# Kernel tuning notes

Measured on AMD Instinct MI355X. Metric: run time of the kernel, lower is better.

## Reference

```python
import jax, jax.numpy as jnp
import numpy as np

B, S, HID = 2, 2048, 2048
H, D = 16, 128
BASE = 10000.0
NEG = -1e9


def _rope_tables(seq_len, dim, dtype):
    inv_freq = 1.0 / (BASE ** (jnp.arange(0, dim, 2, dtype=jnp.float32) / dim))
    pos = jnp.arange(seq_len, dtype=jnp.float32)
    freqs = jnp.einsum('s,d->sd', pos, inv_freq)          # [S, D/2]
    emb = jnp.concatenate([freqs, freqs], axis=-1)        # [S, D]
    return jnp.cos(emb).astype(dtype), jnp.sin(emb).astype(dtype)


def _rotate_half(x):
    x1, x2 = jnp.split(x, 2, axis=-1)
    return jnp.concatenate([-x2, x1], axis=-1)


def setup_inputs() -> dict:
    key = jax.random.key(0)
    k1, k2, k3 = jax.random.split(key, 3)
    x = jax.random.normal(k1, (B, S, HID), dtype=jnp.float32)
    w_qkv = jax.random.normal(k2, (HID, 3 * HID), dtype=jnp.float32) * (HID ** -0.5)
    w_out = jax.random.normal(k3, (HID, HID), dtype=jnp.float32) * (HID ** -0.5)
    return {"x": x, "w_qkv": w_qkv, "w_out": w_out}


def reference(x, w_qkv, w_out):
    b, s, _ = x.shape
    qkv = x @ w_qkv                                        # [B, S, 3*HID]
    qkv = qkv.reshape(b, s, 3, H, D).transpose(2, 0, 3, 1, 4)  # [3, B, H, S, D]
    q, k, v = qkv[0], qkv[1], qkv[2]
    cos, sin = _rope_tables(s, D, x.dtype)                 # [S, D]
    cos = cos[None, None]
    sin = sin[None, None]
    q = q * cos + _rotate_half(q) * sin
    k = k * cos + _rotate_half(k) * sin
    scale = 1.0 / np.sqrt(D)
    scores = jnp.einsum('bhqd,bhkd->bhqk', q, k) * scale   # [B, H, S, S]
    causal = jnp.triu(jnp.ones((s, s), dtype=bool), k=1)
    scores = jnp.where(causal[None, None], NEG, scores)
    attn = jax.nn.softmax(scores, axis=-1)
    out = jnp.einsum('bhqk,bhkd->bhqd', attn, v)           # [B, H, S, D]
    out = out.transpose(0, 2, 1, 3).reshape(b, s, H * D)
    return out @ w_out
```

## Files before the change

### kernel.cpp

```cpp
#include <hip/hip_runtime.h>
#include <hip/hip_bf16.h>

#define S_LEN 2048
#define HID_DIM 2048
#define NH 16
#define HD 128
#define N3 6144

typedef __bf16 bf16x8 __attribute__((ext_vector_type(8)));
typedef unsigned short u16x8 __attribute__((ext_vector_type(8)));
typedef float f32x4 __attribute__((ext_vector_type(4)));
typedef float f32x16 __attribute__((ext_vector_type(16)));

#define MFMA16(a, b, c) __builtin_amdgcn_mfma_f32_16x16x32_bf16(a, b, c, 0, 0, 0)
#define MFMA32(a, b, c) __builtin_amdgcn_mfma_f32_32x32x16_bf16(a, b, c, 0, 0, 0)

__device__ __forceinline__ unsigned short f2bf(float f) {
  union { float f; unsigned u; } v; v.f = f;
  return (unsigned short)((v.u + 0x7fffu + ((v.u >> 16) & 1u)) >> 16);
}
__device__ __forceinline__ float bf2f(unsigned short h) {
  union { unsigned u; float f; } v; v.u = ((unsigned)h) << 16; return v.f;
}
__device__ __forceinline__ unsigned packbf2(float lo, float hi) {
  union { __hip_bfloat162 h2; unsigned u; } cv;
  cv.h2 = __float22bfloat162_rn(make_float2(lo, hi));
  return cv.u;
}
__device__ __forceinline__ void store_c(float* p, float v) { *p = v; }
__device__ __forceinline__ void store_c(unsigned short* p, float v) { *p = f2bf(v); }

__device__ __forceinline__ void async16(const void* g, void* l) {
  __builtin_amdgcn_global_load_lds((const __attribute__((address_space(1))) unsigned int*)g,
                                   (__attribute__((address_space(3))) unsigned int*)l,
                                   16, 0, 0);
}

template <int N> __device__ __forceinline__ void vmcnt();
template <> __device__ __forceinline__ void vmcnt<0>() { asm volatile("s_waitcnt vmcnt(0)" ::: "memory"); }
template <> __device__ __forceinline__ void vmcnt<5>() { asm volatile("s_waitcnt vmcnt(5)" ::: "memory"); }
template <> __device__ __forceinline__ void vmcnt<6>() { asm volatile("s_waitcnt vmcnt(6)" ::: "memory"); }

#define PLSWAP(a, b) asm volatile("v_permlane32_swap_b32 %0, %1" : "+v"(a), "+v"(b))

__global__ __launch_bounds__(256) void prep_all(const float4* __restrict__ x4,
                                                ushort4* __restrict__ xb4,
                                                const float* __restrict__ w_qkv,
                                                unsigned short* __restrict__ wqkvT,
                                                const float* __restrict__ w_out,
                                                unsigned short* __restrict__ woutT,
                                                float* __restrict__ cosT,
                                                float* __restrict__ sinT) {
  __shared__ float t[32][33];
  int bid = blockIdx.x;
  const int tid = threadIdx.x;

  if (bid < 8192) {
    int i = bid * 256 + tid;
    float4 v = x4[i];
    ushort4 o;
    o.x = f2bf(v.x); o.y = f2bf(v.y); o.z = f2bf(v.z); o.w = f2bf(v.w);
    xb4[i] = o;
    return;
  }
  bid -= 8192;
  if (bid < 12288 + 4096) {
    const float* src; unsigned short* dst; int R, Ccols;
    if (bid < 12288) { src = w_qkv; dst = wqkvT; R = 2048; Ccols = 6144; }
    else { bid -= 12288; src = w_out; dst = woutT; R = 2048; Ccols = 2048; }
    int ct = Ccols >> 5;
    int bx = bid % ct, by = bid / ct;
    int c0 = bx << 5, r0 = by << 5;
    int lx = tid & 31, ly = tid >> 5;
#pragma unroll
    for (int i = 0; i < 32; i += 8)
      t[ly + i][lx] = src[(long long)(r0 + ly + i) * Ccols + c0 + lx];
    __syncthreads();
#pragma unroll
    for (int i = 0; i < 32; i += 8)
      dst[(long long)(c0 + ly + i) * R + r0 + lx] = f2bf(t[lx][ly + i]);
    return;
  }
  bid -= 16384;
  int idx = bid * 256 + tid;
  int s = idx >> 6, i = idx & 63;
  float invf = powf(10000.0f, -(float)i * (1.0f / 64.0f));
  float a = (float)s * invf;
  cosT[idx] = cosf(a);
  sinT[idx] = sinf(a);
}

__global__ __launch_bounds__(512) void gemm256(const unsigned short* __restrict__ A,
                                               const unsigned short* __restrict__ Bt,
                                               unsigned short* __restrict__ C,
                                               int Mdim, int Ncols, int ldc, int Kdim) {
  constexpr int AEL = 256 * 64, BUFE = 2 * AEL;
  __shared__ unsigned short smem[2 * BUFE];

  const int ntn = Ncols >> 8;
  const int nwg = (Mdim >> 8) * ntn;
  int bid = blockIdx.x;
  bid = (bid & 7) * (nwg >> 3) + (bid >> 3);
  const int tm = (bid / ntn) << 8;
  const int tn = (bid % ntn) << 8;

  const int tid = threadIdx.x;
  const int w = tid >> 6, l = tid & 63;
  const int g = l >> 4, cc = l & 15;
  const int wm = w >> 2, wn = w & 3;

  const int srow = tid >> 3;
  const int schunk = (tid & 7) ^ (srow & 7);
  const unsigned short* gA = A + (long long)(tm + srow) * Kdim + schunk * 8;
  const unsigned short* gB = Bt + (long long)(tn + srow) * Kdim + schunk * 8;

  const int ch0 = ((g) ^ (cc & 7)) << 3;
  const int ch1 = ((4 + g) ^ (cc & 7)) << 3;

  f32x4 acc[8][4] = {};
  bf16x8 a[4][2], b[4][2];
  const int nk = Kdim >> 6;

#define ST_A(kt2, BUF, s) \
  async16(gA + (long long)(s) * 64 * Kdim + ((long long)(kt2) << 6), \
          smem + (BUF) * BUFE + (s) * 4096 + w * 512)
#define ST_B(kt2, BUF, s) \
  async16(gB + (long long)(s) * 64 * Kdim + ((long long)(kt2) << 6), \
          smem + (BUF) * BUFE + AEL + (s) * 4096 + w * 512)

#pragma unroll
  for (int s = 0; s < 4; ++s) ST_A(0, 0, s);
#pragma unroll
  for (int s = 0; s < 4; ++s) ST_B(0, 0, s);
  ST_A(1, 1, 0); ST_A(1, 1, 2);
  ST_B(1, 1, 0); ST_B(1, 1, 1); ST_B(1, 1, 2); ST_B(1, 1, 3);
  vmcnt<6>();
  __builtin_amdgcn_s_barrier();

#define KSTEP(kt, BUF, OBUF)                                                      \
  {                                                                               \
    const unsigned short* Ab = smem + (BUF) * BUFE + wm * (128 * 64);             \
    const unsigned short* Bb = smem + (BUF) * BUFE + AEL + wn * (64 * 64);        \
                    \
    _Pragma("unroll") for (int i = 0; i < 4; ++i) {                               \
      const int r = (i * 16 + cc) << 6;                                           \
      a[i][0] = *(const bf16x8*)(Ab + r + ch0);                                   \
      a[i][1] = *(const bf16x8*)(Ab + r + ch1);                                   \
    }                                                                             \
    _Pragma("unroll") for (int j = 0; j < 2; ++j) {                               \
      const int r = (j * 16 + cc) << 6;                                           \
      b[j][0] = *(const bf16x8*)(Bb + r + ch0);                                   \
      b[j][1] = *(const bf16x8*)(Bb + r + ch1);                                   \
    }                                                                             \
    if ((kt) + 1 < nk) { ST_A((kt) + 1, OBUF, 1); ST_A((kt) + 1, OBUF, 3); }      \
    __builtin_amdgcn_s_barrier();                                                 \
    __builtin_amdgcn_s_setprio(1);                                                \
    _Pragma("unroll") for (int i = 0; i < 4; ++i)                                 \
      _Pragma("unroll") for (int j = 0; j < 2; ++j) {                             \
        acc[i][j] = MFMA16(a[i][0], b[j][0], acc[i][j]);                          \
        acc[i][j] = MFMA16(a[i][1], b[j][1], acc[i][j]);                          \
      }                                                                           \
    __builtin_amdgcn_s_setprio(0);                                                \
    __builtin_amdgcn_s_barrier();                                                 \
                                              \
    _Pragma("unroll") for (int j = 0; j < 2; ++j) {                               \
      const int r = ((2 + j) * 16 + cc) << 6;                                     \
      b[2 + j][0] = *(const bf16x8*)(Bb + r + ch0);                               \
      b[2 + j][1] = *(const bf16x8*)(Bb + r + ch1);                               \
    }                                                                             \
    if ((kt) + 2 < nk) { ST_A((kt) + 2, BUF, 0); ST_A((kt) + 2, BUF, 2); }        \
    __builtin_amdgcn_s_barrier();                                                 \
    __builtin_amdgcn_s_setprio(1);                                                \
    _Pragma("unroll") for (int i = 0; i < 4; ++i)                                 \
      _Pragma("unroll") for (int j = 0; j < 2; ++j) {                             \
        acc[i][2 + j] = MFMA16(a[i][0], b[2 + j][0], acc[i][2 + j]);              \
        acc[i][2 + j] = MFMA16(a[i][1], b[2 + j][1], acc[i][2 + j]);              \
      }                                                                           \
    __builtin_amdgcn_s_setprio(0);                                                \
    __builtin_amdgcn_s_barrier();                                                 \
                                              \
    _Pragma("unroll") for (int i = 0; i < 4; ++i) {                               \
      const int r = ((64 + i * 16 + cc) << 6);                                    \
      a[i][0] = *(const bf16x8*)(Ab + r + ch0);                                   \
      a[i][1] = *(const bf16x8*)(Ab + r + ch1);                                   \
    }                                                                             \
    if ((kt) + 2 < nk) { ST_B((kt) + 2, BUF, 0); ST_B((kt) + 2, BUF, 1); }        \
    __builtin_amdgcn_s_barrier();                                                 \
    __builtin_amdgcn_s_setprio(1);                                                \
    _Pragma("unroll") for (int i = 0; i < 4; ++i)                                 \
      _Pragma("unroll") for (int j = 0; j < 2; ++j) {                             \
        acc[4 + i][j] = MFMA16(a[i][0], b[j][0], acc[4 + i][j]);                  \
        acc[4 + i][j] = MFMA16(a[i][1], b[j][1], acc[4 + i][j]);                  \
      }                                                                           \
    __builtin_amdgcn_s_setprio(0);                                                \
    __builtin_amdgcn_s_barrier();                                                 \
                            \
    if ((kt) + 2 < nk) { ST_B((kt) + 2, BUF, 2); ST_B((kt) + 2, BUF, 3); }        \
    __builtin_amdgcn_s_barrier();                                                 \
    __builtin_amdgcn_s_setprio(1);                                                \
    _Pragma("unroll") for (int i = 0; i < 4; ++i)                                 \
      _Pragma("unroll") for (int j = 0; j < 2; ++j) {                             \
        acc[4 + i][2 + j] = MFMA16(a[i][0], b[2 + j][0], acc[4 + i][2 + j]);      \
        acc[4 + i][2 + j] = MFMA16(a[i][1], b[2 + j][1], acc[4 + i][2 + j]);      \
      }                                                                           \
    __builtin_amdgcn_s_setprio(0);                                                \
    if ((kt) + 2 < nk) vmcnt<6>(); else vmcnt<0>();                               \
    __builtin_amdgcn_s_barrier();                                                 \
  }

  for (int kt = 0; kt < nk; kt += 2) {
    KSTEP(kt, 0, 1);
    KSTEP(kt + 1, 1, 0);
  }
#undef KSTEP
#undef ST_A
#undef ST_B

  const int crow0 = tm + wm * 128;
  const int ccol0 = tn + wn * 64;
#pragma unroll
  for (int i = 0; i < 8; ++i)
#pragma unroll
    for (int j = 0; j < 4; ++j)
#pragma unroll
      for (int p = 0; p < 4; ++p) {
        int row = crow0 + i * 16 + (g << 2) + p;
        int col = ccol0 + j * 16 + cc;
        store_c(&C[(long long)row * ldc + col], acc[i][j][p]);
      }
}

template <int BM, int BN, typename OutT>
__global__ __launch_bounds__(512) void gemm_pipe8(const unsigned short* __restrict__ A,
                                                  const unsigned short* __restrict__ Bt,
                                                  OutT* __restrict__ C,
                                                  int Mdim, int Ncols, int ldc, int Kdim) {
  constexpr int WTM = BM / 2, WTN = BN / 4;
  constexpr int MREP = WTM / 16, NREP = WTN / 16;
  constexpr int AEL = BM * 64, BEL = BN * 64, BUFE = AEL + BEL;
  constexpr int AINST = BM / 64, BINST = BN / 64;
  constexpr int AHALF = BM / 128, BHALF = BN / 128;
  constexpr int VN = BN / 64 + BM / 128;
  __shared__ unsigned short smem[2 * BUFE];

  const int ntn = Ncols / BN;
  const int nwg = (Mdim / BM) * ntn;
  int bid = blockIdx.x;
  bid = (bid & 7) * (nwg >> 3) + (bid >> 3);
  const int tm = (bid / ntn) * BM;
  const int tn = (bid % ntn) * BN;

  const int tid = threadIdx.x;
  const int w = tid >> 6, l = tid & 63;
  const int g = l >> 4, cc = l & 15;
  const int wm = w >> 2, wn = w & 3;

  const int srow = tid >> 3;
  const int schunk = (tid & 7) ^ (srow & 7);
  const unsigned short* gA = A + (long long)(tm + srow) * Kdim + schunk * 8;
  const unsigned short* gB = Bt + (long long)(tn + srow) * Kdim + schunk * 8;

  const int ch0 = ((g) ^ (cc & 7)) << 3;
  const int ch1 = ((4 + g) ^ (cc & 7)) << 3;

  f32x4 acc[MREP][NREP] = {};
  bf16x8 a[MREP / 2][2], b[NREP][2];

  const int nk = Kdim >> 6;

#define STAGE_A(kt2, s) \
  async16(gA + (long long)(s) * 64 * Kdim + ((long long)(kt2) << 6), \
          smem + ((kt2) & 1) * BUFE + (s) * 4096 + w * 512)
#define STAGE_B(kt2, s) \
  async16(gB + (long long)(s) * 64 * Kdim + ((long long)(kt2) << 6), \
          smem + ((kt2) & 1) * BUFE + AEL + (s) * 4096 + w * 512)

#pragma unroll
  for (int s = 0; s < AINST; ++s) STAGE_A(0, s);
#pragma unroll
  for (int s = 0; s < BINST; ++s) STAGE_B(0, s);
#pragma unroll
  for (int s = 0; s < BINST; ++s) STAGE_B(1, s);
#pragma unroll
  for (int s = 0; s < AHALF; ++s) STAGE_A(1, s);
  vmcnt<VN>();
  __builtin_amdgcn_s_barrier();

  for (int kt = 0; kt < nk; ++kt) {
    const int buf = kt & 1;
    const unsigned short* Ab = smem + buf * BUFE + (wm * WTM) * 64;
    const unsigned short* Bb = smem + buf * BUFE + AEL + (wn * WTN) * 64;

#pragma unroll
    for (int i = 0; i < MREP / 2; ++i) {
      const int r = (i * 16 + cc) << 6;
      a[i][0] = *(const bf16x8*)(Ab + r + ch0);
      a[i][1] = *(const bf16x8*)(Ab + r + ch1);
    }
#pragma unroll
    for (int j = 0; j < NREP; ++j) {
      const int r = (j * 16 + cc) << 6;
      b[j][0] = *(const bf16x8*)(Bb + r + ch0);
      b[j][1] = *(const bf16x8*)(Bb + r + ch1);
    }
    if (kt + 1 < nk) {
#pragma unroll
      for (int s = AHALF; s < AINST; ++s) STAGE_A(kt + 1, s);
    }
    __builtin_amdgcn_s_barrier();
    __builtin_amdgcn_s_setprio(1);
#pragma unroll
    for (int i = 0; i < MREP / 2; ++i)
#pragma unroll
      for (int j = 0; j < NREP / 2; ++j) {
        acc[i][j] = MFMA16(a[i][0], b[j][0], acc[i][j]);
        acc[i][j] = MFMA16(a[i][1], b[j][1], acc[i][j]);
      }
    __builtin_amdgcn_s_setprio(0);
    __builtin_amdgcn_s_barrier();

    if (kt + 2 < nk) {
#pragma unroll
      for (int s = 0; s < BHALF; ++s) STAGE_B(kt + 2, s);
    }
    __builtin_amdgcn_s_barrier();
    __builtin_amdgcn_s_setprio(1);
#pragma unroll
    for (int i = 0; i < MREP / 2; ++i)
#pragma unroll
      for (int j = 0; j < NREP / 2; ++j) {
        f32x4& ac = acc[i][NREP / 2 + j];
        ac = MFMA16(a[i][0], b[NREP / 2 + j][0], ac);
        ac = MFMA16(a[i][1], b[NREP / 2 + j][1], ac);
      }
    __builtin_amdgcn_s_setprio(0);
    __builtin_amdgcn_s_barrier();

#pragma unroll
    for (int i = 0; i < MREP / 2; ++i) {
      const int r = ((WTM / 2) + i * 16 + cc) << 6;
      a[i][0] = *(const bf16x8*)(Ab + r + ch0);
      a[i][1] = *(const bf16x8*)(Ab + r + ch1);
    }
    if (kt + 2 < nk) {
#pragma unroll
      for (int s = BHALF; s < BINST; ++s) STAGE_B(kt + 2, s);
    }
    __builtin_amdgcn_s_barrier();
    __builtin_amdgcn_s_setprio(1);
#pragma unroll
    for (int i = 0; i < MREP / 2; ++i)
#pragma unroll
      for (int j = 0; j < NREP / 2; ++j) {
        f32x4& ac = acc[MREP / 2 + i][j];
        ac = MFMA16(a[i][0], b[j][0], ac);
        ac = MFMA16(a[i][1], b[j][1], ac);
      }
    __builtin_amdgcn_s_setprio(0);
    __builtin_amdgcn_s_barrier();

    if (kt + 2 < nk) {
#pragma unroll
      for (int s = 0; s < AHALF; ++s) STAGE_A(kt + 2, s);
    }
    __builtin_amdgcn_s_barrier();
    __builtin_amdgcn_s_setprio(1);
#pragma unroll
    for (int i = 0; i < MREP / 2; ++i)
#pragma unroll
      for (int j = 0; j < NREP / 2; ++j) {
        f32x4& ac = acc[MREP / 2 + i][NREP / 2 + j];
        ac = MFMA16(a[i][0], b[NREP / 2 + j][0], ac);
        ac = MFMA16(a[i][1], b[NREP / 2 + j][1], ac);
      }
    __builtin_amdgcn_s_setprio(0);
    if (kt + 2 < nk) vmcnt<VN>(); else vmcnt<0>();
    __builtin_amdgcn_s_barrier();
  }
#undef STAGE_A
#undef STAGE_B

  const int crow0 = tm + wm * WTM;
  const int ccol0 = tn + wn * WTN;
#pragma unroll
  for (int i = 0; i < MREP; ++i)
#pragma unroll
    for (int j = 0; j < NREP; ++j)
#pragma unroll
      for (int p = 0; p < 4; ++p) {
        int row = crow0 + i * 16 + (g << 2) + p;
        int col = ccol0 + j * 16 + cc;
        store_c(&C[(long long)row * ldc + col], acc[i][j][p]);
      }
}

__global__ __launch_bounds__(256) void split_rope(const unsigned short* __restrict__ qkv,
                                                  const float* __restrict__ cosT,
                                                  const float* __restrict__ sinT,
                                                  unsigned short* __restrict__ Qb,
                                                  unsigned short* __restrict__ Kb,
                                                  unsigned short* __restrict__ Vt) {
  __shared__ unsigned short vtile[32][128];
  const int bid = blockIdx.x;
  const int st = bid & 63;
  const int h = (bid >> 6) & 15;
  const int b = bid >> 10;
  const int s0 = st << 5;
  const int t = threadIdx.x;
  const float qscale = 0.08838834764831845f;

  {
    const int sl = t >> 3;
    const int d0 = (t & 7) << 3;
    const int s = s0 + sl;
    const long long rb = ((long long)(b * S_LEN + s)) * N3 + h * HD;
    u16x8 qlo = *(const u16x8*)(qkv + rb + d0);
    u16x8 qhi = *(const u16x8*)(qkv + rb + 64 + d0);
    u16x8 klo = *(const u16x8*)(qkv + rb + HID_DIM + d0);
    u16x8 khi = *(const u16x8*)(qkv + rb + HID_DIM + 64 + d0);
    const float* cp = cosT + (s << 6) + d0;
    const float* sp = sinT + (s << 6) + d0;
    f32x4 c0 = *(const f32x4*)(cp), c1 = *(const f32x4*)(cp + 4);
    f32x4 sn0 = *(const f32x4*)(sp), sn1 = *(const f32x4*)(sp + 4);
    u16x8 qo_lo, qo_hi, ko_lo, ko_hi;
#pragma unroll
    for (int j = 0; j < 8; ++j) {
      float cv = (j < 4) ? c0[j & 3] : c1[j & 3];
      float sv = (j < 4) ? sn0[j & 3] : sn1[j & 3];
      float ql = bf2f(qlo[j]), qh = bf2f(qhi[j]);
      float kl = bf2f(klo[j]), kh = bf2f(khi[j]);
      qo_lo[j] = f2bf((ql * cv - qh * sv) * qscale);
      qo_hi[j] = f2bf((qh * cv + ql * sv) * qscale);
      ko_lo[j] = f2bf(kl * cv - kh * sv);
      ko_hi[j] = f2bf(kh * cv + kl * sv);
    }
    const long long ob = ((long long)((b * NH + h) * S_LEN + s)) * HD + d0;
    *(u16x8*)(Qb + ob) = qo_lo;
    *(u16x8*)(Qb + ob + 64) = qo_hi;
    *(u16x8*)(Kb + ob) = ko_lo;
    *(u16x8*)(Kb + ob + 64) = ko_hi;
  }

  {
    const int sl = t >> 3;
    const int d0 = (t & 7) << 4;
    const int s = s0 + sl;
    const long long vb_in = ((long long)(b * S_LEN + s)) * N3 + h * HD + 2 * HID_DIM;
    u16x8 v0 = *(const u16x8*)(qkv + vb_in + d0);
    u16x8 v1 = *(const u16x8*)(qkv + vb_in + d0 + 8);
    *(u16x8*)(&vtile[sl][d0]) = v0;
    *(u16x8*)(&vtile[sl][d0 + 8]) = v1;
  }
  __syncthreads();
  {
    const int dr = t >> 1;
    const int sh = (t & 1) << 4;
    unsigned short tv[16];
#pragma unroll
    for (int j = 0; j < 16; ++j) tv[j] = vtile[sh + j][dr];
    uint4 u0, u1;
    u0.x = (unsigned)tv[0] | ((unsigned)tv[1] << 16);
    u0.y = (unsigned)tv[2] | ((unsigned)tv[3] << 16);
    u0.z = (unsigned)tv[4] | ((unsigned)tv[5] << 16);
    u0.w = (unsigned)tv[6] | ((unsigned)tv[7] << 16);
    u1.x = (unsigned)tv[8] | ((unsigned)tv[9] << 16);
    u1.y = (unsigned)tv[10] | ((unsigned)tv[11] << 16);
    u1.z = (unsigned)tv[12] | ((unsigned)tv[13] << 16);
    u1.w = (unsigned)tv[14] | ((unsigned)tv[15] << 16);
    const long long vb = ((long long)((b * NH + h) * HD + dr)) * S_LEN + s0 + sh;
    *(uint4*)(Vt + vb) = u0;
    *(uint4*)(Vt + vb + 8) = u1;
  }
}

__global__ __launch_bounds__(256) void flash_attn(const unsigned short* __restrict__ Qg,
                                                  const unsigned short* __restrict__ Kg,
                                                  const unsigned short* __restrict__ Vt,
                                                  unsigned short* __restrict__ Ob) {
  __shared__ unsigned short smem[32768];
  const int id = blockIdx.x;
  const int bh = id & 31;
  const int qtr = (id >> 5) & 7;
  const int qt = (id >> 8) ? qtr : 15 - qtr;
  const int Q0 = qt << 7;
  const int b = bh >> 4, h = bh & 15;
  const long long base = (long long)bh * (S_LEN * HD);
  const int tid = threadIdx.x, w = tid >> 6, l = tid & 63;
  const int hi = l >> 5, q = l & 31;
  const int q0w = Q0 + (w << 5);
  const int g = l >> 4, c = l & 15;

  bf16x8 qf[8];
  {
    const unsigned short* qp = Qg + base + (long long)(q0w + q) * HD + (hi << 3);
#pragma unroll
    for (int s = 0; s < 8; ++s) qf[s] = *(const bf16x8*)(qp + (s << 4));
  }

  f32x16 oacc[4] = {};
  float m = -1e30f, lsum = 0.f;

  const int nt = (qt << 1) + 2;

  auto STAGE = [&](int kv0, int buf) {
    unsigned short* ks = smem + buf * 8192;
    unsigned short* vs = smem + 16384 + buf * 8192;
#pragma unroll
    for (int j = 0; j < 4; ++j) {
      int row = (w << 4) + (j << 2) + g;
      int chunk = c ^ (row & 7);
      async16(Kg + base + (long long)(kv0 + row) * HD + (chunk << 3),
              ks + (((w << 4) + (j << 2)) << 7));
    }
#pragma unroll
    for (int j = 0; j < 4; ++j) {
      int dr = (w << 5) + (j << 3) + (l >> 3);
      int chunk = (l & 7) ^ (dr & 7);
      async16(Vt + base + (long long)dr * S_LEN + kv0 + (chunk << 3),
              vs + (((w << 5) + (j << 3)) << 6));
    }
  };

  STAGE(0, 0);
  __syncthreads();

  int cur = 0;
  for (int t = 0; t < nt; ++t) {
    const int kv0 = t << 6;
    if (t + 1 < nt) STAGE((t + 1) << 6, cur ^ 1);

    if (kv0 < q0w + 32) {
      const unsigned short* ks = smem + cur * 8192;
      const unsigned short* vs = smem + 16384 + cur * 8192;

      f32x16 sa[2] = {};
#pragma unroll
      for (int h2 = 0; h2 < 2; ++h2) {
        const char* kb = (const char*)ks + (((h2 << 5) + q) << 8);
        const int r7 = q & 7;
#pragma unroll
        for (int s = 0; s < 8; ++s) {
          bf16x8 kf = *(const bf16x8*)(kb + ((((s << 1) + hi) ^ r7) << 4));
          sa[h2] = MFMA32(kf, qf[s], sa[h2]);
        }
      }

      if (kv0 + 63 > q0w) {
        const int qq = q0w + q;
#pragma unroll
        for (int h2 = 0; h2 < 2; ++h2)
#pragma unroll
          for (int j = 0; j < 16; ++j) {
            int kv = kv0 + (h2 << 5) + (j & 3) + ((j >> 2) << 3) + (hi << 2);
            if (kv > qq) sa[h2][j] = -1e30f;
          }
      }

      float t0 = sa[0][0], t1 = sa[0][1], t2 = sa[0][2], t3 = sa[0][3];
#pragma unroll
      for (int j = 4; j < 16; j += 4) {
        t0 = fmaxf(t0, sa[0][j]);     t1 = fmaxf(t1, sa[0][j + 1]);
        t2 = fmaxf(t2, sa[0][j + 2]); t3 = fmaxf(t3, sa[0][j + 3]);
      }
#pragma unroll
      for (int j = 0; j < 16; j += 4) {
        t0 = fmaxf(t0, sa[1][j]);     t1 = fmaxf(t1, sa[1][j + 1]);
        t2 = fmaxf(t2, sa[1][j + 2]); t3 = fmaxf(t3, sa[1][j + 3]);
      }
      float tmax = fmaxf(fmaxf(t0, t1), fmaxf(t2, t3));
      {
        float tcp;
        asm volatile("v_mov_b32 %0, %1" : "=v"(tcp) : "v"(tmax));
        PLSWAP(tmax, tcp);
        tmax = fmaxf(tmax, tcp);
      }
      float mn = fmaxf(m, tmax);
      float fsc = __expf(m - mn);
      m = mn;
      float s0 = 0.f, s1 = 0.f, s2 = 0.f, s3 = 0.f;
#pragma unroll
      for (int h2 = 0; h2 < 2; ++h2)
#pragma unroll
        for (int j = 0; j < 16; j += 4) {
          float p0 = __expf(sa[h2][j] - mn);
          float p1 = __expf(sa[h2][j + 1] - mn);
          float p2 = __expf(sa[h2][j + 2] - mn);
          float p3 = __expf(sa[h2][j + 3] - mn);
          sa[h2][j] = p0; sa[h2][j + 1] = p1;
          sa[h2][j + 2] = p2; sa[h2][j + 3] = p3;
          s0 += p0; s1 += p1; s2 += p2; s3 += p3;
        }
      float ps = (s0 + s1) + (s2 + s3);
      {
        float pcp;
        asm volatile("v_mov_b32 %0, %1" : "=v"(pcp) : "v"(ps));
        PLSWAP(ps, pcp);
        ps = ps + pcp;
      }
      lsum = lsum * fsc + ps;
#pragma unroll
      for (int db = 0; db < 4; ++db)
#pragma unroll
        for (int j = 0; j < 16; ++j) oacc[db][j] *= fsc;

      unsigned up[2][8];
#pragma unroll
      for (int h2 = 0; h2 < 2; ++h2)
#pragma unroll
        for (int k = 0; k < 8; ++k)
          up[h2][k] = packbf2(sa[h2][2 * k], sa[h2][2 * k + 1]);
      union Frag { unsigned u[4]; bf16x8 v; } pf[4];
#pragma unroll
      for (int s = 0; s < 4; ++s) {
        int h2 = s >> 1, q4 = (s & 1) << 2;
        unsigned a0 = up[h2][q4 + 0], b0 = up[h2][q4 + 2];
        unsigned a1 = up[h2][q4 + 1], b1 = up[h2][q4 + 3];
        PLSWAP(a0, b0);
        PLSWAP(a1, b1);
        pf[s].u[0] = a0; pf[s].u[1] = a1;
        pf[s].u[2] = b0; pf[s].u[3] = b1;
      }

#pragma unroll
      for (int db = 0; db < 4; ++db) {
        const char* vb = (const char*)vs + (((db << 5) + q) << 7);
        const int d7 = q & 7;
#pragma unroll
        for (int s = 0; s < 4; ++s) {
          bf16x8 vf = *(const bf16x8*)(vb + ((((s << 1) + hi) ^ d7) << 4));
          oacc[db] = MFMA32(vf, pf[s].v, oacc[db]);
        }
      }
    }

    __syncthreads();
    cur ^= 1;
  }

  const float rl = 1.0f / lsum;
#pragma unroll
  for (int db = 0; db < 4; ++db)
#pragma unroll
    for (int jg = 0; jg < 4; ++jg) {
      int d = (db << 5) + (jg << 3) + (hi << 2);
      unsigned v0 = packbf2(oacc[db][4 * jg] * rl, oacc[db][4 * jg + 1] * rl);
      unsigned v1 = packbf2(oacc[db][4 * jg + 2] * rl, oacc[db][4 * jg + 3] * rl);
      *(uint2*)(smem + (((w << 5) + q) << 7) + d) = make_uint2(v0, v1);
    }
  __syncthreads();
  {
    const int qr = tid >> 1;
    const int dh = (tid & 1) << 6;
    const uint4* src = (const uint4*)(smem + (qr << 7) + dh);
    uint4* dst = (uint4*)(Ob + (long long)((b << 11) + Q0 + qr) * HID_DIM + (h << 7) + dh);
#pragma unroll
    for (int cc2 = 0; cc2 < 8; ++cc2) dst[cc2] = src[cc2];
  }
}

extern "C" void kernel_launch(void* const* d_in, const int* in_sizes, int n_in,
                              void* d_out, int out_size, void* d_ws, size_t ws_size,
                              hipStream_t stream) {
  (void)in_sizes; (void)n_in; (void)out_size; (void)ws_size;
  const float* x = (const float*)d_in[0];
  const float* w_qkv = (const float*)d_in[1];
  const float* w_out = (const float*)d_in[2];
  float* out = (float*)d_out;
  char* ws = (char*)d_ws;

  unsigned short* xb    = (unsigned short*)(ws);
  unsigned short* wqkvT = (unsigned short*)(ws + 16777216);
  unsigned short* woutT = (unsigned short*)(ws + 41943040);
  unsigned short* qkv   = (unsigned short*)(ws + 50331648);
  unsigned short* Qb    = (unsigned short*)(ws + 100663296);
  unsigned short* Kb    = (unsigned short*)(ws + 117440512);
  unsigned short* Vt    = (unsigned short*)(ws + 134217728);
  float* cosT = (float*)(ws + 150994944);
  float* sinT = (float*)(ws + 151519232);
  unsigned short* Ob = qkv;

  prep_all<<<25088, 256, 0, stream>>>((const float4*)x, (ushort4*)xb,
                                      w_qkv, wqkvT, w_out, woutT, cosT, sinT);
  gemm256<<<256, 512, 0, stream>>>(xb, wqkvT, qkv, 4096, 4096, 6144, 2048);
  gemm_pipe8<128, 256, unsigned short><<<256, 512, 0, stream>>>(
      xb, wqkvT + (long long)4096 * 2048, qkv + 4096, 4096, 2048, 6144, 2048);
  split_rope<<<2048, 256, 0, stream>>>(qkv, cosT, sinT, Qb, Kb, Vt);
  flash_attn<<<512, 256, 0, stream>>>(Qb, Kb, Vt, Ob);
  gemm_pipe8<128, 256, float><<<256, 512, 0, stream>>>(Ob, woutT, out, 4096, 2048, 2048, 2048);
}
```

Baseline: 265.9 us.

## Write V transposed directly from QKV GEMM epilogue and widen K smem swizzle

The V-projection GEMM now stores its output straight into the transposed per-head Vt layout from its epilogue, so split_rope no longer reads V, stages it in shared memory and transposes it. This removes a round trip of V through global memory and an LDS transpose. The epilogue writes 4-element strided chunks, which may coalesce less well. The K tile's shared-memory XOR swizzle is also widened from 8 to 16 chunks to reduce bank conflicts on the K fragment reads.

```diff
diff --git a/kernel.cpp b/kernel.cpp
--- a/kernel.cpp
+++ b/kernel.cpp
@@ -230,7 +230,7 @@
       }
 }
 
-template <int BM, int BN, typename OutT>
+template <int BM, int BN, typename OutT, bool VTOUT = false>
 __global__ __launch_bounds__(512) void gemm_pipe8(const unsigned short* __restrict__ A,
                                                   const unsigned short* __restrict__ Bt,
                                                   OutT* __restrict__ C,
@@ -382,25 +382,40 @@
 
   const int crow0 = tm + wm * WTM;
   const int ccol0 = tn + wn * WTN;
-#pragma unroll
-  for (int i = 0; i < MREP; ++i)
-#pragma unroll
-    for (int j = 0; j < NREP; ++j)
-#pragma unroll
-      for (int p = 0; p < 4; ++p) {
-        int row = crow0 + i * 16 + (g << 2) + p;
+  if constexpr (VTOUT) {
+    unsigned short* Vt = (unsigned short*)C;
+#pragma unroll
+    for (int i = 0; i < MREP; ++i)
+#pragma unroll
+      for (int j = 0; j < NREP; ++j) {
         int col = ccol0 + j * 16 + cc;
-        store_c(&C[(long long)row * ldc + col], acc[i][j][p]);
-      }
+        int rowb = crow0 + i * 16 + (g << 2);
+        long long vt = ((long long)(((rowb >> 11) << 4) + (col >> 7)) * 128 + (col & 127)) * 2048 +
+                       (rowb & 2047);
+        ushort4 o;
+        o.x = f2bf(acc[i][j][0]); o.y = f2bf(acc[i][j][1]);
+        o.z = f2bf(acc[i][j][2]); o.w = f2bf(acc[i][j][3]);
+        *(ushort4*)(Vt + vt) = o;
+      }
+  } else {
+#pragma unroll
+    for (int i = 0; i < MREP; ++i)
+#pragma unroll
+      for (int j = 0; j < NREP; ++j)
+#pragma unroll
+        for (int p = 0; p < 4; ++p) {
+          int row = crow0 + i * 16 + (g << 2) + p;
+          int col = ccol0 + j * 16 + cc;
+          store_c(&C[(long long)row * ldc + col], acc[i][j][p]);
+        }
+  }
 }
 
 __global__ __launch_bounds__(256) void split_rope(const unsigned short* __restrict__ qkv,
                                                   const float* __restrict__ cosT,
                                                   const float* __restrict__ sinT,
                                                   unsigned short* __restrict__ Qb,
-                                                  unsigned short* __restrict__ Kb,
-                                                  unsigned short* __restrict__ Vt) {
-  __shared__ unsigned short vtile[32][128];
+                                                  unsigned short* __restrict__ Kb) {
   const int bid = blockIdx.x;
   const int st = bid & 63;
   const int h = (bid >> 6) & 15;
@@ -409,68 +424,35 @@
   const int t = threadIdx.x;
   const float qscale = 0.08838834764831845f;
 
-  {
-    const int sl = t >> 3;
-    const int d0 = (t & 7) << 3;
-    const int s = s0 + sl;
-    const long long rb = ((long long)(b * S_LEN + s)) * N3 + h * HD;
-    u16x8 qlo = *(const u16x8*)(qkv + rb + d0);
-    u16x8 qhi = *(const u16x8*)(qkv + rb + 64 + d0);
-    u16x8 klo = *(const u16x8*)(qkv + rb + HID_DIM + d0);
-    u16x8 khi = *(const u16x8*)(qkv + rb + HID_DIM + 64 + d0);
-    const float* cp = cosT + (s << 6) + d0;
-    const float* sp = sinT + (s << 6) + d0;
-    f32x4 c0 = *(const f32x4*)(cp), c1 = *(const f32x4*)(cp + 4);
-    f32x4 sn0 = *(const f32x4*)(sp), sn1 = *(const f32x4*)(sp + 4);
-    u16x8 qo_lo, qo_hi, ko_lo, ko_hi;
-#pragma unroll
-    for (int j = 0; j < 8; ++j) {
-      float cv = (j < 4) ? c0[j & 3] : c1[j & 3];
-      float sv = (j < 4) ? sn0[j & 3] : sn1[j & 3];
-      float ql = bf2f(qlo[j]), qh = bf2f(qhi[j]);
-      float kl = bf2f(klo[j]), kh = bf2f(khi[j]);
-      qo_lo[j] = f2bf((ql * cv - qh * sv) * qscale);
-      qo_hi[j] = f2bf((qh * cv + ql * sv) * qscale);
-      ko_lo[j] = f2bf(kl * cv - kh * sv);
-      ko_hi[j] = f2bf(kh * cv + kl * sv);
-    }
-    const long long ob = ((long long)((b * NH + h) * S_LEN + s)) * HD + d0;
-    *(u16x8*)(Qb + ob) = qo_lo;
-    *(u16x8*)(Qb + ob + 64) = qo_hi;
-    *(u16x8*)(Kb + ob) = ko_lo;
-    *(u16x8*)(Kb + ob + 64) = ko_hi;
-  }
-
-  {
-    const int sl = t >> 3;
-    const int d0 = (t & 7) << 4;
-    const int s = s0 + sl;
-    const long long vb_in = ((long long)(b * S_LEN + s)) * N3 + h * HD + 2 * HID_DIM;
-    u16x8 v0 = *(const u16x8*)(qkv + vb_in + d0);
-    u16x8 v1 = *(const u16x8*)(qkv + vb_in + d0 + 8);
-    *(u16x8*)(&vtile[sl][d0]) = v0;
-    *(u16x8*)(&vtile[sl][d0 + 8]) = v1;
-  }
-  __syncthreads();
-  {
-    const int dr = t >> 1;
-    const int sh = (t & 1) << 4;
-    unsigned short tv[16];
-#pragma unroll
-    for (int j = 0; j < 16; ++j) tv[j] = vtile[sh + j][dr];
-    uint4 u0, u1;
-    u0.x = (unsigned)tv[0] | ((unsigned)tv[1] << 16);
-    u0.y = (unsigned)tv[2] | ((unsigned)tv[3] << 16);
-    u0.z = (unsigned)tv[4] | ((unsigned)tv[5] << 16);
-    u0.w = (unsigned)tv[6] | ((unsigned)tv[7] << 16);
-    u1.x = (unsigned)tv[8] | ((unsigned)tv[9] << 16);
-    u1.y = (unsigned)tv[10] | ((unsigned)tv[11] << 16);
-    u1.z = (unsigned)tv[12] | ((unsigned)tv[13] << 16);
-    u1.w = (unsigned)tv[14] | ((unsigned)tv[15] << 16);
-    const long long vb = ((long long)((b * NH + h) * HD + dr)) * S_LEN + s0 + sh;
-    *(uint4*)(Vt + vb) = u0;
-    *(uint4*)(Vt + vb + 8) = u1;
-  }
+  const int sl = t >> 3;
+  const int d0 = (t & 7) << 3;
+  const int s = s0 + sl;
+  const long long rb = ((long long)(b * S_LEN + s)) * N3 + h * HD;
+  u16x8 qlo = *(const u16x8*)(qkv + rb + d0);
+  u16x8 qhi = *(const u16x8*)(qkv + rb + 64 + d0);
+  u16x8 klo = *(const u16x8*)(qkv + rb + HID_DIM + d0);
+  u16x8 khi = *(const u16x8*)(qkv + rb + HID_DIM + 64 + d0);
+  const float* cp = cosT + (s << 6) + d0;
+  const float* sp = sinT + (s << 6) + d0;
+  f32x4 c0 = *(const f32x4*)(cp), c1 = *(const f32x4*)(cp + 4);
+  f32x4 sn0 = *(const f32x4*)(sp), sn1 = *(const f32x4*)(sp + 4);
+  u16x8 qo_lo, qo_hi, ko_lo, ko_hi;
+#pragma unroll
+  for (int j = 0; j < 8; ++j) {
+    float cv = (j < 4) ? c0[j & 3] : c1[j & 3];
+    float sv = (j < 4) ? sn0[j & 3] : sn1[j & 3];
+    float ql = bf2f(qlo[j]), qh = bf2f(qhi[j]);
+    float kl = bf2f(klo[j]), kh = bf2f(khi[j]);
+    qo_lo[j] = f2bf((ql * cv - qh * sv) * qscale);
+    qo_hi[j] = f2bf((qh * cv + ql * sv) * qscale);
+    ko_lo[j] = f2bf(kl * cv - kh * sv);
+    ko_hi[j] = f2bf(kh * cv + kl * sv);
+  }
+  const long long ob = ((long long)((b * NH + h) * S_LEN + s)) * HD + d0;
+  *(u16x8*)(Qb + ob) = qo_lo;
+  *(u16x8*)(Qb + ob + 64) = qo_hi;
+  *(u16x8*)(Kb + ob) = ko_lo;
+  *(u16x8*)(Kb + ob + 64) = ko_hi;
 }
 
 __global__ __launch_bounds__(256) void flash_attn(const unsigned short* __restrict__ Qg,
@@ -508,7 +490,7 @@
 #pragma unroll
     for (int j = 0; j < 4; ++j) {
       int row = (w << 4) + (j << 2) + g;
-      int chunk = c ^ (row & 7);
+      int chunk = c ^ (row & 15);
       async16(Kg + base + (long long)(kv0 + row) * HD + (chunk << 3),
               ks + (((w << 4) + (j << 2)) << 7));
     }
@@ -537,10 +519,10 @@
 #pragma unroll
       for (int h2 = 0; h2 < 2; ++h2) {
         const char* kb = (const char*)ks + (((h2 << 5) + q) << 8);
-        const int r7 = q & 7;
+        const int rm = q & 15;
 #pragma unroll
         for (int s = 0; s < 8; ++s) {
-          bf16x8 kf = *(const bf16x8*)(kb + ((((s << 1) + hi) ^ r7) << 4));
+          bf16x8 kf = *(const bf16x8*)(kb + ((((s << 1) + hi) ^ rm) << 4));
           sa[h2] = MFMA32(kf, qf[s], sa[h2]);
         }
       }
@@ -682,9 +664,9 @@
   prep_all<<<25088, 256, 0, stream>>>((const float4*)x, (ushort4*)xb,
                                       w_qkv, wqkvT, w_out, woutT, cosT, sinT);
   gemm256<<<256, 512, 0, stream>>>(xb, wqkvT, qkv, 4096, 4096, 6144, 2048);
-  gemm_pipe8<128, 256, unsigned short><<<256, 512, 0, stream>>>(
-      xb, wqkvT + (long long)4096 * 2048, qkv + 4096, 4096, 2048, 6144, 2048);
-  split_rope<<<2048, 256, 0, stream>>>(qkv, cosT, sinT, Qb, Kb, Vt);
+  gemm_pipe8<128, 256, unsigned short, true><<<256, 512, 0, stream>>>(
+      xb, wqkvT + (long long)4096 * 2048, Vt, 4096, 2048, 2048, 2048);
+  split_rope<<<2048, 256, 0, stream>>>(qkv, cosT, sinT, Qb, Kb);
   flash_attn<<<512, 256, 0, stream>>>(Qb, Kb, Vt, Ob);
   gemm_pipe8<128, 256, float><<<256, 512, 0, stream>>>(Ob, woutT, out, 4096, 2048, 2048, 2048);
 }
```

New measurement: 261.1 us. About the same (-1.8%).
